# Kernel optimization log

Hardware: AMD Instinct MI355X
Metric: run time of the kernel (lower is better)

## Reference

```python
import jax, jax.numpy as jnp
import numpy as np

B, C, H, W = 8, 256, 64, 64
IC = 64  # inter_channels


def conv1x1(x, w, b):
    # x: [B,C,H,W], w: [O,C], b: [O]
    return jnp.einsum('bchw,oc->bohw', x, w) + b[None, :, None, None]


def maxpool2(x):
    # 2x2 max pool, stride 2. x: [B,C,H,W]
    b, c, h, w = x.shape
    return x.reshape(b, c, h // 2, 2, w // 2, 2).max(axis=(3, 5))


def setup_inputs() -> dict:
    key = jax.random.key(0)
    ks = jax.random.split(key, 9)
    s_in = 1.0 / np.sqrt(C)
    s_ic = 1.0 / np.sqrt(IC)
    return {
        'x': jax.random.normal(ks[0], (B, C, H, W), dtype=jnp.float32),
        'g_w': jax.random.uniform(ks[1], (IC, C), jnp.float32, -s_in, s_in),
        'g_b': jax.random.uniform(ks[2], (IC,), jnp.float32, -s_in, s_in),
        'theta_w': jax.random.uniform(ks[3], (IC, C), jnp.float32, -s_in, s_in),
        'theta_b': jax.random.uniform(ks[4], (IC,), jnp.float32, -s_in, s_in),
        'phi_w': jax.random.uniform(ks[5], (IC, C), jnp.float32, -s_in, s_in),
        'phi_b': jax.random.uniform(ks[6], (IC,), jnp.float32, -s_in, s_in),
        'W_w': jax.random.uniform(ks[7], (C, IC), jnp.float32, -np.sqrt(6.0 / IC), np.sqrt(6.0 / IC)),
        'W_b': jax.random.uniform(ks[8], (C,), jnp.float32, -s_ic, s_ic),
    }


def reference(x, g_w, g_b, theta_w, theta_b, phi_w, phi_b, W_w, W_b):
    b, c, h, w = x.shape
    n = h * w                     # query positions
    m = (h // 2) * (w // 2)       # pooled key/value positions

    v = maxpool2(conv1x1(x, g_w, g_b)).reshape(b, IC, m).transpose(0, 2, 1)   # [b,m,ic]
    q = conv1x1(x, theta_w, theta_b).reshape(b, IC, n).transpose(0, 2, 1)     # [b,n,ic]
    k = maxpool2(conv1x1(x, phi_w, phi_b)).reshape(b, IC, m)                  # [b,ic,m]

    attn = jax.nn.softmax(jnp.einsum('bni,bim->bnm', q, k), axis=-1)          # [b,n,m]
    attended = jnp.einsum('bnm,bmi->bni', attn, v)                            # [b,n,ic]
    attended = attended.transpose(0, 2, 1).reshape(b, IC, h, w)
    # F.interpolate to (h,w) is identity here: attended already has spatial (h,w)
    return conv1x1(attended, W_w, W_b) + x
```

## Files before the change

### kernel.cpp

```cpp
#include <hip/hip_runtime.h>

typedef unsigned short ushort_t;
typedef unsigned int   uint_t;

typedef __attribute__((ext_vector_type(8))) short  short8;
typedef __attribute__((ext_vector_type(4))) short  short4v;
typedef __attribute__((ext_vector_type(4))) float  float4v;

#define BB    8
#define CC    256
#define HH    64
#define WW2   64
#define NPIX  4096
#define MPOS  1024
#define ICH   64

__device__ __forceinline__ float bf2f(ushort_t u) {
  return __uint_as_float(((uint_t)u) << 16);
}
__device__ __forceinline__ ushort_t f2bf(float f) {
  uint_t i = __float_as_uint(f);
  uint_t r = (i + 0x7FFFu + ((i >> 16) & 1u)) >> 16;
  return (ushort_t)r;
}
__device__ __forceinline__ uint_t pack2(float a, float b) {
  return (uint_t)f2bf(a) | ((uint_t)f2bf(b) << 16);
}

__global__ __launch_bounds__(256) void prep_kernel(
    const float* __restrict__ theta_w, const float* __restrict__ phi_w,
    const float* __restrict__ g_w, const float* __restrict__ W_w,
    const float* __restrict__ theta_b, const float* __restrict__ phi_b,
    const float* __restrict__ g_b,
    ushort_t* __restrict__ wAll, ushort_t* __restrict__ Wbf,
    float* __restrict__ biasAll) {
  int i = blockIdx.x * 256 + threadIdx.x;
  if (i < 16384)        wAll[i] = f2bf(theta_w[i]);
  else if (i < 32768)   wAll[i] = f2bf(phi_w[i - 16384]);
  else if (i < 49152)   wAll[i] = f2bf(g_w[i - 32768]);
  else if (i < 65536)   Wbf[i - 49152] = f2bf(W_w[i - 49152]);
  else if (i < 65600)   biasAll[i - 65536] = theta_b[i - 65536];
  else if (i < 65664)   biasAll[i - 65536] = phi_b[i - 65600];
  else if (i < 65728)   biasAll[i - 65536] = g_b[i - 65664];
}

__global__ __launch_bounds__(256, 2) void qkv_kernel(
    const float* __restrict__ x, const ushort_t* __restrict__ wAll,
    const float* __restrict__ biasAll,
    ushort_t* __restrict__ qbuf, ushort_t* __restrict__ kTbuf,
    ushort_t* __restrict__ vTbuf) {
  __shared__ __align__(16) ushort_t Bs[2][64 * 64];
  int tid = threadIdx.x;
  int wave = tid >> 6, lane = tid & 63;
  int quad = lane >> 4, col = lane & 15;
  int b = blockIdx.x >> 6, tile = blockIdx.x & 63;
  int r2 = tile >> 1, chalf = tile & 1;
  const float* xb = x + (size_t)b * (CC * NPIX) + (r2 * 2) * WW2 + chalf * 32;

  int sp = tid & 63;
  int cq = tid >> 6;
  int goff = (sp >> 5) * WW2 + (sp & 31);

  float4v acc[3][4];
#pragma unroll
  for (int ot = 0; ot < 3; ++ot) {
    int ob = wave * 48 + ot * 16 + quad * 4;
    float4v bv;
#pragma unroll
    for (int r = 0; r < 4; ++r) bv[r] = biasAll[ob + r];
#pragma unroll
    for (int s = 0; s < 4; ++s) acc[ot][s] = bv;
  }

  float st[16];

#define LOAD_CHUNK(kc)                                                     \
  {                                                                        \
    _Pragma("unroll") for (int j = 0; j < 16; ++j)                         \
      st[j] = xb[((kc) * 64 + cq * 16 + j) * NPIX + goff];                 \
  }
#define WRITE_CHUNK(buf)                                                   \
  {                                                                        \
    _Pragma("unroll") for (int u = 0; u < 2; ++u) {                        \
      uint4 w;                                                             \
      w.x = pack2(st[u * 8 + 0], st[u * 8 + 1]);                           \
      w.y = pack2(st[u * 8 + 2], st[u * 8 + 3]);                           \
      w.z = pack2(st[u * 8 + 4], st[u * 8 + 5]);                           \
      w.w = pack2(st[u * 8 + 6], st[u * 8 + 7]);                           \
      *(uint4*)&Bs[(buf)][sp * 64 + (((cq * 2 + u) ^ (sp & 7)) * 8)] = w;  \
    }                                                                      \
  }

  LOAD_CHUNK(0);
  WRITE_CHUNK(0);
  __syncthreads();

  for (int kc = 0; kc < 4; ++kc) {
    if (kc < 3) LOAD_CHUNK(kc + 1);
    int buf = kc & 1;
#pragma unroll
    for (int ksl = 0; ksl < 2; ++ksl) {
      short8 aw[3];
#pragma unroll
      for (int ot = 0; ot < 3; ++ot)
        aw[ot] = *(const short8*)&wAll[(size_t)(wave * 48 + ot * 16 + col) * 256 +
                                       kc * 64 + ksl * 32 + quad * 8];
#pragma unroll
      for (int s = 0; s < 4; ++s) {
        short8 bx = *(const short8*)&Bs[buf][(s * 16 + col) * 64 +
                                             (((ksl * 4 + quad) ^ (col & 7)) * 8)];
#pragma unroll
        for (int ot = 0; ot < 3; ++ot)
          acc[ot][s] = __builtin_amdgcn_mfma_f32_16x16x32_bf16(aw[ot], bx, acc[ot][s], 0, 0, 0);
      }
    }
    if (kc < 3) {
      WRITE_CHUNK((kc + 1) & 1);
      __syncthreads();
    }
  }
#undef LOAD_CHUNK
#undef WRITE_CHUNK

#pragma unroll
  for (int ot = 0; ot < 3; ++ot) {
    int ob = wave * 48 + ot * 16;
    if (ob < 64) {
#pragma unroll
      for (int s = 0; s < 4; ++s) {
        int n = (r2 * 2 + (s >> 1)) * WW2 + chalf * 32 + (s & 1) * 16 + col;
        uint2 u;
        u.x = pack2(acc[ot][s][0], acc[ot][s][1]);
        u.y = pack2(acc[ot][s][2], acc[ot][s][3]);
        *(uint2*)&qbuf[((size_t)(b * NPIX + n)) * ICH + ob + quad * 4] = u;
      }
    } else if (ob < 128) {
#pragma unroll
      for (int s = 0; s < 2; ++s) {
        float4v pm;
#pragma unroll
        for (int r = 0; r < 4; ++r) {
          float v = fmaxf(acc[ot][s][r], acc[ot][s + 2][r]);
          pm[r] = fmaxf(v, __shfl_xor(v, 1));
        }
        if ((lane & 1) == 0) {
          int m = r2 * 32 + chalf * 16 + s * 8 + (col >> 1);
          uint2 u;
          u.x = pack2(pm[0], pm[1]);
          u.y = pack2(pm[2], pm[3]);
          *(uint2*)&kTbuf[((size_t)(b * MPOS + m)) * ICH + (ob - 64) + quad * 4] = u;
        }
      }
    } else {
#pragma unroll
      for (int s = 0; s < 2; ++s) {
        float4v pm;
#pragma unroll
        for (int r = 0; r < 4; ++r) {
          float v = fmaxf(acc[ot][s][r], acc[ot][s + 2][r]);
          pm[r] = fmaxf(v, __shfl_xor(v, 1));
        }
        if ((lane & 1) == 0) {
          int m = r2 * 32 + chalf * 16 + s * 8 + (col >> 1);
#pragma unroll
          for (int r = 0; r < 4; ++r)
            vTbuf[((size_t)(b * ICH + (ob - 128) + quad * 4 + r)) * MPOS + m] = f2bf(pm[r]);
        }
      }
    }
  }
}

__global__ __launch_bounds__(256, 2) void attn_kernel(
    const ushort_t* __restrict__ qbuf, const ushort_t* __restrict__ kTbuf,
    const ushort_t* __restrict__ vTbuf, ushort_t* __restrict__ attbuf) {
  __shared__ __align__(16) ushort_t Ks[2][64 * 64];
  __shared__ __align__(16) ushort_t Vs[2][64 * 64];
  __shared__ __align__(16) ushort_t Ps[64 * 68];
  int tid  = threadIdx.x;
  int wave = tid >> 6, lane = tid & 63;
  int quad = lane >> 4, col = lane & 15;
  int b = blockIdx.x >> 6, qt = blockIdx.x & 63;

  const ushort_t* qrow = qbuf + ((size_t)(b * NPIX + qt * 64 + wave * 16 + col)) * ICH;
  short8 aQ0 = *(const short8*)&qrow[quad * 8];
  short8 aQ1 = *(const short8*)&qrow[32 + quad * 8];

  int krow0 = tid >> 3,           kblk0 = tid & 7;
  int krow1 = (tid + 256) >> 3,   kblk1 = tid & 7;
  int vic = tid >> 2, vseg = tid & 3;

  const uint4* ksrc0 = (const uint4*)(kTbuf + ((size_t)(b * MPOS)) * ICH);
  const ushort_t* vbase = vTbuf + ((size_t)(b * ICH + vic)) * MPOS;

  {
    uint4 k0 = ksrc0[tid], k1 = ksrc0[tid + 256];
    const uint4* vsrc = (const uint4*)(vbase + vseg * 16);
    uint4 v0 = vsrc[0], v1 = vsrc[1];
    *(uint4*)&Ks[0][krow0 * 64 + ((kblk0 ^ (krow0 & 7)) * 8)] = k0;
    *(uint4*)&Ks[0][krow1 * 64 + ((kblk1 ^ (krow1 & 7)) * 8)] = k1;
    *(uint4*)&Vs[0][vic * 64 + (((vseg * 2 + 0) ^ (vic & 7)) * 8)] = v0;
    *(uint4*)&Vs[0][vic * 64 + (((vseg * 2 + 1) ^ (vic & 7)) * 8)] = v1;
  }
  __syncthreads();

  const float4v zero4 = {0.f, 0.f, 0.f, 0.f};
  float l_lane[4] = {0.f, 0.f, 0.f, 0.f};
  float4v o_acc[4];
#pragma unroll
  for (int t = 0; t < 4; ++t) o_acc[t] = zero4;

  for (int kt = 0; kt < 16; ++kt) {
    uint4 nk0, nk1, nv0, nv1;
    if (kt < 15) {
      const uint4* ksrc = (const uint4*)(kTbuf + ((size_t)(b * MPOS + (kt + 1) * 64)) * ICH);
      nk0 = ksrc[tid];
      nk1 = ksrc[tid + 256];
      const uint4* vsrc = (const uint4*)(vbase + (kt + 1) * 64 + vseg * 16);
      nv0 = vsrc[0];
      nv1 = vsrc[1];
    }
    int buf = kt & 1;

    float4v s_acc[4];
#pragma unroll
    for (int t = 0; t < 4; ++t) {
      float4v s = zero4;
      short8 bk0 = *(const short8*)&Ks[buf][(t * 16 + col) * 64 + (((0 * 4 + quad) ^ (col & 7)) * 8)];
      s = __builtin_amdgcn_mfma_f32_16x16x32_bf16(aQ0, bk0, s, 0, 0, 0);
      short8 bk1 = *(const short8*)&Ks[buf][(t * 16 + col) * 64 + (((1 * 4 + quad) ^ (col & 7)) * 8)];
      s = __builtin_amdgcn_mfma_f32_16x16x32_bf16(aQ1, bk1, s, 0, 0, 0);
      s_acc[t] = s;
    }

#pragma unroll
    for (int r = 0; r < 4; ++r) {
      int prow = (wave * 16 + quad * 4 + r) * 68;
#pragma unroll
      for (int t = 0; t < 4; ++t) {
        float pv = __expf(s_acc[t][r]);
        l_lane[r] += pv;
        Ps[prow + t * 16 + col] = f2bf(pv);
      }
    }

#pragma unroll
    for (int kk = 0; kk < 2; ++kk) {
      int pbase = (wave * 16 + col) * 68 + kk * 32 + quad * 8;
      short4v plo = *(const short4v*)&Ps[pbase];
      short4v phi = *(const short4v*)&Ps[pbase + 4];
      short8 ap = __builtin_shufflevector(plo, phi, 0, 1, 2, 3, 4, 5, 6, 7);
#pragma unroll
      for (int t = 0; t < 4; ++t) {
        short8 bv = *(const short8*)&Vs[buf][(t * 16 + col) * 64 + (((kk * 4 + quad) ^ (col & 7)) * 8)];
        o_acc[t] = __builtin_amdgcn_mfma_f32_16x16x32_bf16(ap, bv, o_acc[t], 0, 0, 0);
      }
    }

    if (kt < 15) {
      int nbuf = buf ^ 1;
      *(uint4*)&Ks[nbuf][krow0 * 64 + ((kblk0 ^ (krow0 & 7)) * 8)] = nk0;
      *(uint4*)&Ks[nbuf][krow1 * 64 + ((kblk1 ^ (krow1 & 7)) * 8)] = nk1;
      *(uint4*)&Vs[nbuf][vic * 64 + (((vseg * 2 + 0) ^ (vic & 7)) * 8)] = nv0;
      *(uint4*)&Vs[nbuf][vic * 64 + (((vseg * 2 + 1) ^ (vic & 7)) * 8)] = nv1;
      __syncthreads();
    }
  }

#pragma unroll
  for (int r = 0; r < 4; ++r) {
    float l = l_lane[r];
    l += __shfl_xor(l, 1);
    l += __shfl_xor(l, 2);
    l += __shfl_xor(l, 4);
    l += __shfl_xor(l, 8);
    float inv = 1.0f / l;
    size_t row = ((size_t)(b * NPIX + qt * 64 + wave * 16 + quad * 4 + r)) * ICH;
#pragma unroll
    for (int t = 0; t < 4; ++t)
      attbuf[row + t * 16 + col] = f2bf(o_acc[t][r] * inv);
  }
}

__global__ __launch_bounds__(256, 2) void outconv_kernel(
    const ushort_t* __restrict__ attbuf, const float* __restrict__ x,
    const ushort_t* __restrict__ Wbf, const float* __restrict__ W_b,
    float* __restrict__ out) {
  int tid = threadIdx.x;
  int wave = tid >> 6, lane = tid & 63;
  int quad = lane >> 4, col = lane & 15;
  int b = blockIdx.x >> 6, pt = blockIdx.x & 63;

  float4v acc[4][4];
#pragma unroll
  for (int os = 0; os < 4; ++os) {
    float bv = W_b[wave * 64 + os * 16 + col];
    float4v bvec = {bv, bv, bv, bv};
#pragma unroll
    for (int ps = 0; ps < 4; ++ps) acc[os][ps] = bvec;
  }

  short8 af[2][4];
#pragma unroll
  for (int ps = 0; ps < 4; ++ps)
#pragma unroll
    for (int ks = 0; ks < 2; ++ks)
      af[ks][ps] = *(const short8*)&attbuf[((size_t)(b * NPIX + pt * 64 + ps * 16 + col)) * ICH +
                                           ks * 32 + quad * 8];

#pragma unroll
  for (int os = 0; os < 4; ++os) {
#pragma unroll
    for (int ks = 0; ks < 2; ++ks) {
      short8 wf = *(const short8*)&Wbf[(size_t)(wave * 64 + os * 16 + col) * ICH +
                                       ks * 32 + quad * 8];
#pragma unroll
      for (int ps = 0; ps < 4; ++ps)
        acc[os][ps] = __builtin_amdgcn_mfma_f32_16x16x32_bf16(af[ks][ps], wf, acc[os][ps], 0, 0, 0);
    }
  }

#pragma unroll
  for (int os = 0; os < 4; ++os) {
#pragma unroll
    for (int ps = 0; ps < 4; ++ps) {
      int o = wave * 64 + os * 16 + col;
      int p = pt * 64 + ps * 16 + quad * 4;
      size_t idx = ((size_t)(b * CC + o)) * NPIX + p;
      float4 xv = *(const float4*)&x[idx];
      float4 ov;
      ov.x = acc[os][ps][0] + xv.x;
      ov.y = acc[os][ps][1] + xv.y;
      ov.z = acc[os][ps][2] + xv.z;
      ov.w = acc[os][ps][3] + xv.w;
      *(float4*)&out[idx] = ov;
    }
  }
}

extern "C" void kernel_launch(void* const* d_in, const int* in_sizes, int n_in,
                              void* d_out, int out_size, void* d_ws, size_t ws_size,
                              hipStream_t stream) {
  const float* x       = (const float*)d_in[0];
  const float* g_w     = (const float*)d_in[1];
  const float* g_b     = (const float*)d_in[2];
  const float* theta_w = (const float*)d_in[3];
  const float* theta_b = (const float*)d_in[4];
  const float* phi_w   = (const float*)d_in[5];
  const float* phi_b   = (const float*)d_in[6];
  const float* W_w     = (const float*)d_in[7];
  const float* W_b     = (const float*)d_in[8];
  (void)in_sizes; (void)n_in; (void)out_size; (void)ws_size;

  char* ws = (char*)d_ws;
  ushort_t* wAll    = (ushort_t*)(ws + 0);
  ushort_t* Wbf     = (ushort_t*)(ws + 98304);
  float*    biasAll = (float*)(ws + 131072);
  ushort_t* qbuf    = (ushort_t*)(ws + 262144);
  ushort_t* kTbuf   = (ushort_t*)(ws + 4456448);
  ushort_t* vTbuf   = (ushort_t*)(ws + 5505024);
  ushort_t* attbuf  = (ushort_t*)(ws + 6553600);
  float* out = (float*)d_out;

  prep_kernel<<<257, 256, 0, stream>>>(theta_w, phi_w, g_w, W_w,
                                       theta_b, phi_b, g_b,
                                       wAll, Wbf, biasAll);
  qkv_kernel<<<512, 256, 0, stream>>>(x, wAll, biasAll, qbuf, kTbuf, vTbuf);
  attn_kernel<<<512, 256, 0, stream>>>(qbuf, kTbuf, vTbuf, attbuf);
  outconv_kernel<<<512, 256, 0, stream>>>(attbuf, x, Wbf, W_b, out);
}
```

Before: 135.4 us.

## Pre-transpose x to bf16, split attention keys across waves, double grid sizes

A new prep kernel transposes x into a pixel-major bf16 buffer, so the QKV projection can read MFMA operands straight from global memory with no LDS staging. The attention kernel now gives each block 32 queries, with two wave pairs handling the two key halves; their partial outputs and row sums are combined through shared memory at the end. The QKV, attention and output-conv kernels all launch twice as many smaller blocks with higher occupancy hints. The cost is an extra full pass that writes and re-reads a transposed copy of x, more synchronisation in the attention loop, and the P matrix is now rounded with a cheaper round-half-away mode.

```diff
diff --git a/kernel.cpp b/kernel.cpp
--- a/kernel.cpp
+++ b/kernel.cpp
@@ -23,155 +23,143 @@
   uint_t r = (i + 0x7FFFu + ((i >> 16) & 1u)) >> 16;
   return (ushort_t)r;
 }
+__device__ __forceinline__ ushort_t f2bf_rna(float f) {
+  return (ushort_t)((__float_as_uint(f) + 0x8000u) >> 16);
+}
 __device__ __forceinline__ uint_t pack2(float a, float b) {
   return (uint_t)f2bf(a) | ((uint_t)f2bf(b) << 16);
 }
 
-__global__ __launch_bounds__(256) void prep_kernel(
+__global__ __launch_bounds__(256) void xpose_prep_kernel(
+    const float* __restrict__ x,
     const float* __restrict__ theta_w, const float* __restrict__ phi_w,
     const float* __restrict__ g_w, const float* __restrict__ W_w,
     const float* __restrict__ theta_b, const float* __restrict__ phi_b,
     const float* __restrict__ g_b,
-    ushort_t* __restrict__ wAll, ushort_t* __restrict__ Wbf,
-    float* __restrict__ biasAll) {
-  int i = blockIdx.x * 256 + threadIdx.x;
-  if (i < 16384)        wAll[i] = f2bf(theta_w[i]);
-  else if (i < 32768)   wAll[i] = f2bf(phi_w[i - 16384]);
-  else if (i < 49152)   wAll[i] = f2bf(g_w[i - 32768]);
-  else if (i < 65536)   Wbf[i - 49152] = f2bf(W_w[i - 49152]);
-  else if (i < 65600)   biasAll[i - 65536] = theta_b[i - 65536];
-  else if (i < 65664)   biasAll[i - 65536] = phi_b[i - 65600];
-  else if (i < 65728)   biasAll[i - 65536] = g_b[i - 65664];
-}
-
-__global__ __launch_bounds__(256, 2) void qkv_kernel(
-    const float* __restrict__ x, const ushort_t* __restrict__ wAll,
+    ushort_t* __restrict__ xT, ushort_t* __restrict__ wAll,
+    ushort_t* __restrict__ Wbf, float* __restrict__ biasAll) {
+  int bid = blockIdx.x;
+  int tid = threadIdx.x;
+  if (bid < 2048) {
+    __shared__ __align__(16) ushort_t T[64 * 72];
+    int b = bid >> 8, rest = bid & 255;
+    int ct = rest >> 6, pt = rest & 63;
+    int w = tid >> 6, pl = tid & 63;
+    const float* src = x + ((size_t)(b * CC + ct * 64)) * NPIX + pt * 64;
+#pragma unroll
+    for (int i = 0; i < 16; ++i) {
+      int cl = i * 4 + w;
+      T[pl * 72 + cl] = f2bf(src[(size_t)cl * NPIX + pl]);
+    }
+    __syncthreads();
+#pragma unroll
+    for (int j = 0; j < 2; ++j) {
+      int flat = tid * 2 + j;
+      int p = flat >> 3, seg = flat & 7;
+      uint4 v = *(const uint4*)&T[p * 72 + seg * 8];
+      *(uint4*)&xT[((size_t)(b * NPIX + pt * 64 + p)) * CC + ct * 64 + seg * 8] = v;
+    }
+  } else {
+    int i = (bid - 2048) * 256 + tid;
+    if (i < 16384)        wAll[i] = f2bf(theta_w[i]);
+    else if (i < 32768)   wAll[i] = f2bf(phi_w[i - 16384]);
+    else if (i < 49152)   wAll[i] = f2bf(g_w[i - 32768]);
+    else if (i < 65536)   Wbf[i - 49152] = f2bf(W_w[i - 49152]);
+    else if (i < 65600)   biasAll[i - 65536] = theta_b[i - 65536];
+    else if (i < 65664)   biasAll[i - 65536] = phi_b[i - 65600];
+    else if (i < 65728)   biasAll[i - 65536] = g_b[i - 65664];
+  }
+}
+
+__global__ __launch_bounds__(256, 4) void qkv_kernel(
+    const ushort_t* __restrict__ xT, const ushort_t* __restrict__ wAll,
     const float* __restrict__ biasAll,
     ushort_t* __restrict__ qbuf, ushort_t* __restrict__ kTbuf,
     ushort_t* __restrict__ vTbuf) {
-  __shared__ __align__(16) ushort_t Bs[2][64 * 64];
   int tid = threadIdx.x;
   int wave = tid >> 6, lane = tid & 63;
   int quad = lane >> 4, col = lane & 15;
-  int b = blockIdx.x >> 6, tile = blockIdx.x & 63;
-  int r2 = tile >> 1, chalf = tile & 1;
-  const float* xb = x + (size_t)b * (CC * NPIX) + (r2 * 2) * WW2 + chalf * 32;
-
-  int sp = tid & 63;
-  int cq = tid >> 6;
-  int goff = (sp >> 5) * WW2 + (sp & 31);
-
-  float4v acc[3][4];
+  int b = blockIdx.x >> 7, tile = blockIdx.x & 127;
+  int r2 = tile >> 2, co = tile & 3;
+
+  const ushort_t* brow0 = xT + ((size_t)(b * NPIX + (2 * r2 + 0) * WW2 + co * 16 + col)) * CC;
+  const ushort_t* brow1 = xT + ((size_t)(b * NPIX + (2 * r2 + 1) * WW2 + co * 16 + col)) * CC;
+  const ushort_t* wbase = wAll + (size_t)(wave * 48 + col) * CC;
+
+  float4v acc[3][2];
 #pragma unroll
   for (int ot = 0; ot < 3; ++ot) {
     int ob = wave * 48 + ot * 16 + quad * 4;
     float4v bv;
 #pragma unroll
     for (int r = 0; r < 4; ++r) bv[r] = biasAll[ob + r];
-#pragma unroll
-    for (int s = 0; s < 4; ++s) acc[ot][s] = bv;
-  }
-
-  float st[16];
-
-#define LOAD_CHUNK(kc)                                                     \
-  {                                                                        \
-    _Pragma("unroll") for (int j = 0; j < 16; ++j)                         \
-      st[j] = xb[((kc) * 64 + cq * 16 + j) * NPIX + goff];                 \
-  }
-#define WRITE_CHUNK(buf)                                                   \
-  {                                                                        \
-    _Pragma("unroll") for (int u = 0; u < 2; ++u) {                        \
-      uint4 w;                                                             \
-      w.x = pack2(st[u * 8 + 0], st[u * 8 + 1]);                           \
-      w.y = pack2(st[u * 8 + 2], st[u * 8 + 3]);                           \
-      w.z = pack2(st[u * 8 + 4], st[u * 8 + 5]);                           \
-      w.w = pack2(st[u * 8 + 6], st[u * 8 + 7]);                           \
-      *(uint4*)&Bs[(buf)][sp * 64 + (((cq * 2 + u) ^ (sp & 7)) * 8)] = w;  \
-    }                                                                      \
-  }
-
-  LOAD_CHUNK(0);
-  WRITE_CHUNK(0);
-  __syncthreads();
-
+    acc[ot][0] = bv;
+    acc[ot][1] = bv;
+  }
+
+#pragma unroll
   for (int kc = 0; kc < 4; ++kc) {
-    if (kc < 3) LOAD_CHUNK(kc + 1);
-    int buf = kc & 1;
 #pragma unroll
     for (int ksl = 0; ksl < 2; ++ksl) {
+      int koff = kc * 64 + ksl * 32 + quad * 8;
       short8 aw[3];
 #pragma unroll
       for (int ot = 0; ot < 3; ++ot)
-        aw[ot] = *(const short8*)&wAll[(size_t)(wave * 48 + ot * 16 + col) * 256 +
-                                       kc * 64 + ksl * 32 + quad * 8];
-#pragma unroll
-      for (int s = 0; s < 4; ++s) {
-        short8 bx = *(const short8*)&Bs[buf][(s * 16 + col) * 64 +
-                                             (((ksl * 4 + quad) ^ (col & 7)) * 8)];
-#pragma unroll
-        for (int ot = 0; ot < 3; ++ot)
-          acc[ot][s] = __builtin_amdgcn_mfma_f32_16x16x32_bf16(aw[ot], bx, acc[ot][s], 0, 0, 0);
-      }
-    }
-    if (kc < 3) {
-      WRITE_CHUNK((kc + 1) & 1);
-      __syncthreads();
-    }
-  }
-#undef LOAD_CHUNK
-#undef WRITE_CHUNK
+        aw[ot] = *(const short8*)&wbase[(size_t)(ot * 16) * CC + koff];
+      short8 b0 = *(const short8*)&brow0[koff];
+      short8 b1 = *(const short8*)&brow1[koff];
+#pragma unroll
+      for (int ot = 0; ot < 3; ++ot) {
+        acc[ot][0] = __builtin_amdgcn_mfma_f32_16x16x32_bf16(aw[ot], b0, acc[ot][0], 0, 0, 0);
+        acc[ot][1] = __builtin_amdgcn_mfma_f32_16x16x32_bf16(aw[ot], b1, acc[ot][1], 0, 0, 0);
+      }
+    }
+  }
 
 #pragma unroll
   for (int ot = 0; ot < 3; ++ot) {
     int ob = wave * 48 + ot * 16;
     if (ob < 64) {
 #pragma unroll
-      for (int s = 0; s < 4; ++s) {
-        int n = (r2 * 2 + (s >> 1)) * WW2 + chalf * 32 + (s & 1) * 16 + col;
+      for (int s = 0; s < 2; ++s) {
+        int n = (2 * r2 + s) * WW2 + co * 16 + col;
         uint2 u;
         u.x = pack2(acc[ot][s][0], acc[ot][s][1]);
         u.y = pack2(acc[ot][s][2], acc[ot][s][3]);
         *(uint2*)&qbuf[((size_t)(b * NPIX + n)) * ICH + ob + quad * 4] = u;
       }
     } else if (ob < 128) {
-#pragma unroll
-      for (int s = 0; s < 2; ++s) {
-        float4v pm;
-#pragma unroll
-        for (int r = 0; r < 4; ++r) {
-          float v = fmaxf(acc[ot][s][r], acc[ot][s + 2][r]);
-          pm[r] = fmaxf(v, __shfl_xor(v, 1));
-        }
-        if ((lane & 1) == 0) {
-          int m = r2 * 32 + chalf * 16 + s * 8 + (col >> 1);
-          uint2 u;
-          u.x = pack2(pm[0], pm[1]);
-          u.y = pack2(pm[2], pm[3]);
-          *(uint2*)&kTbuf[((size_t)(b * MPOS + m)) * ICH + (ob - 64) + quad * 4] = u;
-        }
+      float4v pm;
+#pragma unroll
+      for (int r = 0; r < 4; ++r) {
+        float v = fmaxf(acc[ot][0][r], acc[ot][1][r]);
+        pm[r] = fmaxf(v, __shfl_xor(v, 1));
+      }
+      if ((lane & 1) == 0) {
+        int m = r2 * 32 + co * 8 + (col >> 1);
+        uint2 u;
+        u.x = pack2(pm[0], pm[1]);
+        u.y = pack2(pm[2], pm[3]);
+        *(uint2*)&kTbuf[((size_t)(b * MPOS + m)) * ICH + (ob - 64) + quad * 4] = u;
       }
     } else {
-#pragma unroll
-      for (int s = 0; s < 2; ++s) {
-        float4v pm;
-#pragma unroll
-        for (int r = 0; r < 4; ++r) {
-          float v = fmaxf(acc[ot][s][r], acc[ot][s + 2][r]);
-          pm[r] = fmaxf(v, __shfl_xor(v, 1));
-        }
-        if ((lane & 1) == 0) {
-          int m = r2 * 32 + chalf * 16 + s * 8 + (col >> 1);
-#pragma unroll
-          for (int r = 0; r < 4; ++r)
-            vTbuf[((size_t)(b * ICH + (ob - 128) + quad * 4 + r)) * MPOS + m] = f2bf(pm[r]);
-        }
-      }
-    }
-  }
-}
-
-__global__ __launch_bounds__(256, 2) void attn_kernel(
+      float4v pm;
+#pragma unroll
+      for (int r = 0; r < 4; ++r) {
+        float v = fmaxf(acc[ot][0][r], acc[ot][1][r]);
+        pm[r] = fmaxf(v, __shfl_xor(v, 1));
+      }
+      if ((lane & 1) == 0) {
+        int m = r2 * 32 + co * 8 + (col >> 1);
+#pragma unroll
+        for (int r = 0; r < 4; ++r)
+          vTbuf[((size_t)(b * ICH + (ob - 128) + quad * 4 + r)) * MPOS + m] = f2bf(pm[r]);
+      }
+    }
+  }
+}
+
+__global__ __launch_bounds__(256, 3) void attn_kernel(
     const ushort_t* __restrict__ qbuf, const ushort_t* __restrict__ kTbuf,
     const ushort_t* __restrict__ vTbuf, ushort_t* __restrict__ attbuf) {
   __shared__ __align__(16) ushort_t Ks[2][64 * 64];
@@ -180,28 +168,45 @@
   int tid  = threadIdx.x;
   int wave = tid >> 6, lane = tid & 63;
   int quad = lane >> 4, col = lane & 15;
-  int b = blockIdx.x >> 6, qt = blockIdx.x & 63;
-
-  const ushort_t* qrow = qbuf + ((size_t)(b * NPIX + qt * 64 + wave * 16 + col)) * ICH;
+  int wq = wave & 1, wk = wave >> 1;
+  int b = blockIdx.x >> 7, qt = blockIdx.x & 127;
+
+  const ushort_t* qrow = qbuf + ((size_t)(b * NPIX + qt * 32 + wq * 16 + col)) * ICH;
   short8 aQ0 = *(const short8*)&qrow[quad * 8];
   short8 aQ1 = *(const short8*)&qrow[32 + quad * 8];
 
-  int krow0 = tid >> 3,           kblk0 = tid & 7;
-  int krow1 = (tid + 256) >> 3,   kblk1 = tid & 7;
+  int krow0 = tid >> 3, kblk = tid & 7;
+  int krow1 = krow0 + 32;
   int vic = tid >> 2, vseg = tid & 3;
-
-  const uint4* ksrc0 = (const uint4*)(kTbuf + ((size_t)(b * MPOS)) * ICH);
+  const uint4* kbase = (const uint4*)(kTbuf + ((size_t)(b * MPOS)) * ICH);
   const ushort_t* vbase = vTbuf + ((size_t)(b * ICH + vic)) * MPOS;
 
-  {
-    uint4 k0 = ksrc0[tid], k1 = ksrc0[tid + 256];
-    const uint4* vsrc = (const uint4*)(vbase + vseg * 16);
-    uint4 v0 = vsrc[0], v1 = vsrc[1];
-    *(uint4*)&Ks[0][krow0 * 64 + ((kblk0 ^ (krow0 & 7)) * 8)] = k0;
-    *(uint4*)&Ks[0][krow1 * 64 + ((kblk1 ^ (krow1 & 7)) * 8)] = k1;
-    *(uint4*)&Vs[0][vic * 64 + (((vseg * 2 + 0) ^ (vic & 7)) * 8)] = v0;
-    *(uint4*)&Vs[0][vic * 64 + (((vseg * 2 + 1) ^ (vic & 7)) * 8)] = v1;
-  }
+  uint4 pk[4], pv[4];
+#define AT_LOAD(i)                                                          \
+  {                                                                         \
+    const uint4* k0p = kbase + (size_t)(i) * 512;                           \
+    const uint4* k1p = kbase + (size_t)((i) + 8) * 512;                     \
+    pk[0] = k0p[tid]; pk[1] = k0p[tid + 256];                               \
+    pk[2] = k1p[tid]; pk[3] = k1p[tid + 256];                               \
+    const uint4* v0p = (const uint4*)(vbase + (i) * 64);                    \
+    const uint4* v1p = (const uint4*)(vbase + ((i) + 8) * 64);              \
+    pv[0] = v0p[vseg]; pv[1] = v0p[vseg + 4];                               \
+    pv[2] = v1p[vseg]; pv[3] = v1p[vseg + 4];                               \
+  }
+#define AT_WRITE()                                                          \
+  {                                                                         \
+    *(uint4*)&Ks[0][krow0 * 64 + ((kblk ^ (krow0 & 7)) * 8)] = pk[0];       \
+    *(uint4*)&Ks[0][krow1 * 64 + ((kblk ^ (krow1 & 7)) * 8)] = pk[1];       \
+    *(uint4*)&Ks[1][krow0 * 64 + ((kblk ^ (krow0 & 7)) * 8)] = pk[2];       \
+    *(uint4*)&Ks[1][krow1 * 64 + ((kblk ^ (krow1 & 7)) * 8)] = pk[3];       \
+    *(uint4*)&Vs[0][vic * 64 + ((vseg ^ (vic & 7)) * 8)] = pv[0];           \
+    *(uint4*)&Vs[0][vic * 64 + (((vseg + 4) ^ (vic & 7)) * 8)] = pv[1];     \
+    *(uint4*)&Vs[1][vic * 64 + ((vseg ^ (vic & 7)) * 8)] = pv[2];           \
+    *(uint4*)&Vs[1][vic * 64 + (((vseg + 4) ^ (vic & 7)) * 8)] = pv[3];     \
+  }
+
+  AT_LOAD(0);
+  AT_WRITE();
   __syncthreads();
 
   const float4v zero4 = {0.f, 0.f, 0.f, 0.f};
@@ -210,25 +215,16 @@
 #pragma unroll
   for (int t = 0; t < 4; ++t) o_acc[t] = zero4;
 
-  for (int kt = 0; kt < 16; ++kt) {
-    uint4 nk0, nk1, nv0, nv1;
-    if (kt < 15) {
-      const uint4* ksrc = (const uint4*)(kTbuf + ((size_t)(b * MPOS + (kt + 1) * 64)) * ICH);
-      nk0 = ksrc[tid];
-      nk1 = ksrc[tid + 256];
-      const uint4* vsrc = (const uint4*)(vbase + (kt + 1) * 64 + vseg * 16);
-      nv0 = vsrc[0];
-      nv1 = vsrc[1];
-    }
-    int buf = kt & 1;
+  for (int i = 0; i < 8; ++i) {
+    if (i < 7) AT_LOAD(i + 1);
 
     float4v s_acc[4];
 #pragma unroll
     for (int t = 0; t < 4; ++t) {
       float4v s = zero4;
-      short8 bk0 = *(const short8*)&Ks[buf][(t * 16 + col) * 64 + (((0 * 4 + quad) ^ (col & 7)) * 8)];
+      short8 bk0 = *(const short8*)&Ks[wk][(t * 16 + col) * 64 + ((quad ^ (col & 7)) * 8)];
       s = __builtin_amdgcn_mfma_f32_16x16x32_bf16(aQ0, bk0, s, 0, 0, 0);
-      short8 bk1 = *(const short8*)&Ks[buf][(t * 16 + col) * 64 + (((1 * 4 + quad) ^ (col & 7)) * 8)];
+      short8 bk1 = *(const short8*)&Ks[wk][(t * 16 + col) * 64 + (((4 + quad) ^ (col & 7)) * 8)];
       s = __builtin_amdgcn_mfma_f32_16x16x32_bf16(aQ1, bk1, s, 0, 0, 0);
       s_acc[t] = s;
     }
@@ -238,9 +234,9 @@
       int prow = (wave * 16 + quad * 4 + r) * 68;
 #pragma unroll
       for (int t = 0; t < 4; ++t) {
-        float pv = __expf(s_acc[t][r]);
-        l_lane[r] += pv;
-        Ps[prow + t * 16 + col] = f2bf(pv);
+        float pv_ = __expf(s_acc[t][r]);
+        l_lane[r] += pv_;
+        Ps[prow + t * 16 + col] = f2bf_rna(pv_);
       }
     }
 
@@ -252,60 +248,78 @@
       short8 ap = __builtin_shufflevector(plo, phi, 0, 1, 2, 3, 4, 5, 6, 7);
 #pragma unroll
       for (int t = 0; t < 4; ++t) {
-        short8 bv = *(const short8*)&Vs[buf][(t * 16 + col) * 64 + (((kk * 4 + quad) ^ (col & 7)) * 8)];
+        short8 bv = *(const short8*)&Vs[wk][(t * 16 + col) * 64 + (((kk * 4 + quad) ^ (col & 7)) * 8)];
         o_acc[t] = __builtin_amdgcn_mfma_f32_16x16x32_bf16(ap, bv, o_acc[t], 0, 0, 0);
       }
     }
 
-    if (kt < 15) {
-      int nbuf = buf ^ 1;
-      *(uint4*)&Ks[nbuf][krow0 * 64 + ((kblk0 ^ (krow0 & 7)) * 8)] = nk0;
-      *(uint4*)&Ks[nbuf][krow1 * 64 + ((kblk1 ^ (krow1 & 7)) * 8)] = nk1;
-      *(uint4*)&Vs[nbuf][vic * 64 + (((vseg * 2 + 0) ^ (vic & 7)) * 8)] = nv0;
-      *(uint4*)&Vs[nbuf][vic * 64 + (((vseg * 2 + 1) ^ (vic & 7)) * 8)] = nv1;
+    if (i < 7) {
       __syncthreads();
-    }
-  }
-
-#pragma unroll
-  for (int r = 0; r < 4; ++r) {
-    float l = l_lane[r];
-    l += __shfl_xor(l, 1);
-    l += __shfl_xor(l, 2);
-    l += __shfl_xor(l, 4);
-    l += __shfl_xor(l, 8);
-    float inv = 1.0f / l;
-    size_t row = ((size_t)(b * NPIX + qt * 64 + wave * 16 + quad * 4 + r)) * ICH;
+      AT_WRITE();
+      __syncthreads();
+    }
+  }
+#undef AT_LOAD
+#undef AT_WRITE
+
+  __syncthreads();
+  float* S = (float*)Ks;
+  if (wk == 1) {
+    float* dst = S + (size_t)(wq * 64 + lane) * 20;
 #pragma unroll
     for (int t = 0; t < 4; ++t)
-      attbuf[row + t * 16 + col] = f2bf(o_acc[t][r] * inv);
-  }
-}
-
-__global__ __launch_bounds__(256, 2) void outconv_kernel(
+#pragma unroll
+      for (int r = 0; r < 4; ++r) dst[t * 4 + r] = o_acc[t][r];
+#pragma unroll
+    for (int r = 0; r < 4; ++r) dst[16 + r] = l_lane[r];
+  }
+  __syncthreads();
+  if (wk == 0) {
+    const float* srcp = S + (size_t)(wq * 64 + lane) * 20;
+#pragma unroll
+    for (int t = 0; t < 4; ++t)
+#pragma unroll
+      for (int r = 0; r < 4; ++r) o_acc[t][r] += srcp[t * 4 + r];
+#pragma unroll
+    for (int r = 0; r < 4; ++r) {
+      float l = l_lane[r] + srcp[16 + r];
+      l += __shfl_xor(l, 1);
+      l += __shfl_xor(l, 2);
+      l += __shfl_xor(l, 4);
+      l += __shfl_xor(l, 8);
+      float inv = 1.0f / l;
+      size_t row = ((size_t)(b * NPIX + qt * 32 + wq * 16 + quad * 4 + r)) * ICH;
+#pragma unroll
+      for (int t = 0; t < 4; ++t)
+        attbuf[row + t * 16 + col] = f2bf(o_acc[t][r] * inv);
+    }
+  }
+}
+
+__global__ __launch_bounds__(256, 4) void outconv_kernel(
     const ushort_t* __restrict__ attbuf, const float* __restrict__ x,
     const ushort_t* __restrict__ Wbf, const float* __restrict__ W_b,
     float* __restrict__ out) {
   int tid = threadIdx.x;
   int wave = tid >> 6, lane = tid & 63;
   int quad = lane >> 4, col = lane & 15;
-  int b = blockIdx.x >> 6, pt = blockIdx.x & 63;
-
-  float4v acc[4][4];
+  int b = blockIdx.x >> 7, pt = blockIdx.x & 127;
+
+  float4v acc[4][2];
 #pragma unroll
   for (int os = 0; os < 4; ++os) {
     float bv = W_b[wave * 64 + os * 16 + col];
     float4v bvec = {bv, bv, bv, bv};
-#pragma unroll
-    for (int ps = 0; ps < 4; ++ps) acc[os][ps] = bvec;
-  }
-
-  short8 af[2][4];
-#pragma unroll
-  for (int ps = 0; ps < 4; ++ps)
+    acc[os][0] = bvec;
+    acc[os][1] = bvec;
+  }
+
+  short8 af[2][2];
+#pragma unroll
+  for (int ps = 0; ps < 2; ++ps)
 #pragma unroll
     for (int ks = 0; ks < 2; ++ks)
-      af[ks][ps] = *(const short8*)&attbuf[((size_t)(b * NPIX + pt * 64 + ps * 16 + col)) * ICH +
+      af[ks][ps] = *(const short8*)&attbuf[((size_t)(b * NPIX + pt * 32 + ps * 16 + col)) * ICH +
                                            ks * 32 + quad * 8];
 
 #pragma unroll
@@ -314,18 +328,17 @@
     for (int ks = 0; ks < 2; ++ks) {
       short8 wf = *(const short8*)&Wbf[(size_t)(wave * 64 + os * 16 + col) * ICH +
                                        ks * 32 + quad * 8];
-#pragma unroll
-      for (int ps = 0; ps < 4; ++ps)
-        acc[os][ps] = __builtin_amdgcn_mfma_f32_16x16x32_bf16(af[ks][ps], wf, acc[os][ps], 0, 0, 0);
+      acc[os][0] = __builtin_amdgcn_mfma_f32_16x16x32_bf16(af[ks][0], wf, acc[os][0], 0, 0, 0);
+      acc[os][1] = __builtin_amdgcn_mfma_f32_16x16x32_bf16(af[ks][1], wf, acc[os][1], 0, 0, 0);
     }
   }
 
 #pragma unroll
   for (int os = 0; os < 4; ++os) {
 #pragma unroll
-    for (int ps = 0; ps < 4; ++ps) {
+    for (int ps = 0; ps < 2; ++ps) {
       int o = wave * 64 + os * 16 + col;
-      int p = pt * 64 + ps * 16 + quad * 4;
+      int p = pt * 32 + ps * 16 + quad * 4;
       size_t idx = ((size_t)(b * CC + o)) * NPIX + p;
       float4 xv = *(const float4*)&x[idx];
       float4 ov;
@@ -356,16 +369,17 @@
   ushort_t* wAll    = (ushort_t*)(ws + 0);
   ushort_t* Wbf     = (ushort_t*)(ws + 98304);
   float*    biasAll = (float*)(ws + 131072);
-  ushort_t* qbuf    = (ushort_t*)(ws + 262144);
-  ushort_t* kTbuf   = (ushort_t*)(ws + 4456448);
-  ushort_t* vTbuf   = (ushort_t*)(ws + 5505024);
-  ushort_t* attbuf  = (ushort_t*)(ws + 6553600);
+  ushort_t* xT      = (ushort_t*)(ws + 262144);
+  ushort_t* attbuf  = (ushort_t*)(ws + 262144);
+  ushort_t* qbuf    = (ushort_t*)(ws + 17039360);
+  ushort_t* kTbuf   = (ushort_t*)(ws + 21233664);
+  ushort_t* vTbuf   = (ushort_t*)(ws + 22282240);
   float* out = (float*)d_out;
 
-  prep_kernel<<<257, 256, 0, stream>>>(theta_w, phi_w, g_w, W_w,
-                                       theta_b, phi_b, g_b,
-                                       wAll, Wbf, biasAll);
-  qkv_kernel<<<512, 256, 0, stream>>>(x, wAll, biasAll, qbuf, kTbuf, vTbuf);
-  attn_kernel<<<512, 256, 0, stream>>>(qbuf, kTbuf, vTbuf, attbuf);
-  outconv_kernel<<<512, 256, 0, stream>>>(attbuf, x, Wbf, W_b, out);
-}
+  xpose_prep_kernel<<<2305, 256, 0, stream>>>(x, theta_w, phi_w, g_w, W_w,
+                                              theta_b, phi_b, g_b,
+                                              xT, wAll, Wbf, biasAll);
+  qkv_kernel<<<1024, 256, 0, stream>>>(xT, wAll, biasAll, qbuf, kTbuf, vTbuf);
+  attn_kernel<<<1024, 256, 0, stream>>>(qbuf, kTbuf, vTbuf, attbuf);
+  outconv_kernel<<<1024, 256, 0, stream>>>(attbuf, x, Wbf, W_b, out);
+}
```

Result: slower. 210.4 us (+55.4%).

## Pre-transpose x to pixel-major bf16 and re-tile qkv and outconv kernels

Applied to the files above, without the earlier changes.

A new prep kernel transposes x into a pixel-major bf16 buffer and stores the weights in a k-block-interleaved layout. The qkv kernel then loads a whole 64x256 tile into LDS with coalesced 16-byte loads instead of strided fp32 gathers. It raises occupancy to 4 blocks per SM, and the output conv uses smaller 32-pixel tiles across twice as many blocks. Softmax probabilities now use a cheaper round-to-nearest bf16 conversion. The trade-off is an extra full read and write of x through the transpose buffer.

```diff
diff --git a/kernel.cpp b/kernel.cpp
--- a/kernel.cpp
+++ b/kernel.cpp
@@ -23,43 +23,85 @@
   uint_t r = (i + 0x7FFFu + ((i >> 16) & 1u)) >> 16;
   return (ushort_t)r;
 }
+__device__ __forceinline__ ushort_t f2bf_rna(float f) {
+  return (ushort_t)((__float_as_uint(f) + 0x8000u) >> 16);
+}
 __device__ __forceinline__ uint_t pack2(float a, float b) {
   return (uint_t)f2bf(a) | ((uint_t)f2bf(b) << 16);
 }
 
-__global__ __launch_bounds__(256) void prep_kernel(
+__global__ __launch_bounds__(256) void xpose_prep_kernel(
+    const float* __restrict__ x,
     const float* __restrict__ theta_w, const float* __restrict__ phi_w,
     const float* __restrict__ g_w, const float* __restrict__ W_w,
     const float* __restrict__ theta_b, const float* __restrict__ phi_b,
     const float* __restrict__ g_b,
-    ushort_t* __restrict__ wAll, ushort_t* __restrict__ Wbf,
-    float* __restrict__ biasAll) {
-  int i = blockIdx.x * 256 + threadIdx.x;
-  if (i < 16384)        wAll[i] = f2bf(theta_w[i]);
-  else if (i < 32768)   wAll[i] = f2bf(phi_w[i - 16384]);
-  else if (i < 49152)   wAll[i] = f2bf(g_w[i - 32768]);
-  else if (i < 65536)   Wbf[i - 49152] = f2bf(W_w[i - 49152]);
-  else if (i < 65600)   biasAll[i - 65536] = theta_b[i - 65536];
-  else if (i < 65664)   biasAll[i - 65536] = phi_b[i - 65600];
-  else if (i < 65728)   biasAll[i - 65536] = g_b[i - 65664];
-}
-
-__global__ __launch_bounds__(256, 2) void qkv_kernel(
-    const float* __restrict__ x, const ushort_t* __restrict__ wAll,
+    ushort_t* __restrict__ xT, ushort_t* __restrict__ wA2,
+    ushort_t* __restrict__ Wbf2, float* __restrict__ biasAll) {
+  int bid = blockIdx.x;
+  int tid = threadIdx.x;
+  if (bid < 2048) {
+    __shared__ __align__(16) ushort_t T[64 * 72];
+    int b = bid >> 8, rest = bid & 255;
+    int ct = rest >> 6, pt = rest & 63;
+    int w = tid >> 6, pl = tid & 63;
+    const float* src = x + ((size_t)(b * CC + ct * 64)) * NPIX + pt * 64;
+#pragma unroll
+    for (int i = 0; i < 16; ++i) {
+      int cl = i * 4 + w;
+      T[pl * 72 + cl] = f2bf(src[(size_t)cl * NPIX + pl]);
+    }
+    __syncthreads();
+#pragma unroll
+    for (int j = 0; j < 2; ++j) {
+      int flat = tid * 2 + j;
+      int p = flat >> 3, seg = flat & 7;
+      uint4 v = *(const uint4*)&T[p * 72 + seg * 8];
+      *(uint4*)&xT[((size_t)(b * NPIX + pt * 64 + p)) * CC + ct * 64 + seg * 8] = v;
+    }
+  } else {
+    int i = (bid - 2048) * 256 + tid;
+    if (i < 49152) {
+      float v = (i < 16384) ? theta_w[i]
+              : (i < 32768) ? phi_w[i - 16384]
+                            : g_w[i - 32768];
+      int o = i >> 8, c = i & 255;
+      wA2[(c >> 3) * 1536 + o * 8 + (c & 7)] = f2bf(v);
+    } else if (i < 65536) {
+      int j = i - 49152;
+      int o = j >> 6, ic = j & 63;
+      Wbf2[(ic >> 3) * 2048 + o * 8 + (ic & 7)] = f2bf(W_w[j]);
+    } else if (i < 65600)    biasAll[i - 65536] = theta_b[i - 65536];
+    else if (i < 65664)      biasAll[i - 65536] = phi_b[i - 65600];
+    else if (i < 65728)      biasAll[i - 65536] = g_b[i - 65664];
+  }
+}
+
+__global__ __launch_bounds__(256, 4) void qkv_kernel(
+    const ushort_t* __restrict__ xT, const ushort_t* __restrict__ wA2,
     const float* __restrict__ biasAll,
     ushort_t* __restrict__ qbuf, ushort_t* __restrict__ kTbuf,
     ushort_t* __restrict__ vTbuf) {
-  __shared__ __align__(16) ushort_t Bs[2][64 * 64];
+  __shared__ __align__(16) ushort_t Bsu[64 * 256];
+  uint4* Bs16 = (uint4*)Bsu;
   int tid = threadIdx.x;
   int wave = tid >> 6, lane = tid & 63;
   int quad = lane >> 4, col = lane & 15;
-  int b = blockIdx.x >> 6, tile = blockIdx.x & 63;
-  int r2 = tile >> 1, chalf = tile & 1;
-  const float* xb = x + (size_t)b * (CC * NPIX) + (r2 * 2) * WW2 + chalf * 32;
-
-  int sp = tid & 63;
-  int cq = tid >> 6;
-  int goff = (sp >> 5) * WW2 + (sp & 31);
+  int b = blockIdx.x >> 6, t = blockIdx.x & 63;
+  int rj = t >> 1, h = t & 1;
+
+  const uint4* src0 = (const uint4*)(xT + ((size_t)(b * NPIX + (2 * rj + 0) * WW2 + h * 32)) * CC);
+  const uint4* src1 = (const uint4*)(xT + ((size_t)(b * NPIX + (2 * rj + 1) * WW2 + h * 32)) * CC);
+
+#pragma unroll
+  for (int it = 0; it < 8; ++it) {
+    int g = it * 256 + tid;
+    int chunk = g >> 10, off = g & 1023;
+    int lp = chunk * 32 + (off >> 5), j = off & 31;
+    uint4 v = (chunk == 0) ? src0[off] : src1[off];
+    Bs16[lp * 32 + (j & ~7) + ((j & 7) ^ (lp & 7))] = v;
+  }
+  __syncthreads();
 
   float4v acc[3][4];
 #pragma unroll
@@ -72,55 +114,26 @@
     for (int s = 0; s < 4; ++s) acc[ot][s] = bv;
   }
 
-  float st[16];
-
-#define LOAD_CHUNK(kc)                                                     \
-  {                                                                        \
-    _Pragma("unroll") for (int j = 0; j < 16; ++j)                         \
-      st[j] = xb[((kc) * 64 + cq * 16 + j) * NPIX + goff];                 \
-  }
-#define WRITE_CHUNK(buf)                                                   \
-  {                                                                        \
-    _Pragma("unroll") for (int u = 0; u < 2; ++u) {                        \
-      uint4 w;                                                             \
-      w.x = pack2(st[u * 8 + 0], st[u * 8 + 1]);                           \
-      w.y = pack2(st[u * 8 + 2], st[u * 8 + 3]);                           \
-      w.z = pack2(st[u * 8 + 4], st[u * 8 + 5]);                           \
-      w.w = pack2(st[u * 8 + 6], st[u * 8 + 7]);                           \
-      *(uint4*)&Bs[(buf)][sp * 64 + (((cq * 2 + u) ^ (sp & 7)) * 8)] = w;  \
-    }                                                                      \
-  }
-
-  LOAD_CHUNK(0);
-  WRITE_CHUNK(0);
-  __syncthreads();
-
-  for (int kc = 0; kc < 4; ++kc) {
-    if (kc < 3) LOAD_CHUNK(kc + 1);
-    int buf = kc & 1;
-#pragma unroll
-    for (int ksl = 0; ksl < 2; ++ksl) {
-      short8 aw[3];
+  const uint4* wA16 = (const uint4*)wA2;
+#pragma unroll
+  for (int ks = 0; ks < 8; ++ks) {
+    int kblk = ks * 4 + quad;
+    short8 aw[3];
+#pragma unroll
+    for (int ot = 0; ot < 3; ++ot) {
+      uint4 a = wA16[kblk * 192 + wave * 48 + ot * 16 + col];
+      aw[ot] = *(const short8*)&a;
+    }
+#pragma unroll
+    for (int s = 0; s < 4; ++s) {
+      int lp = s * 16 + col;
+      uint4 braw = Bs16[lp * 32 + (kblk & ~7) + ((kblk & 7) ^ (lp & 7))];
+      short8 bx = *(const short8*)&braw;
 #pragma unroll
       for (int ot = 0; ot < 3; ++ot)
-        aw[ot] = *(const short8*)&wAll[(size_t)(wave * 48 + ot * 16 + col) * 256 +
-                                       kc * 64 + ksl * 32 + quad * 8];
-#pragma unroll
-      for (int s = 0; s < 4; ++s) {
-        short8 bx = *(const short8*)&Bs[buf][(s * 16 + col) * 64 +
-                                             (((ksl * 4 + quad) ^ (col & 7)) * 8)];
-#pragma unroll
-        for (int ot = 0; ot < 3; ++ot)
-          acc[ot][s] = __builtin_amdgcn_mfma_f32_16x16x32_bf16(aw[ot], bx, acc[ot][s], 0, 0, 0);
-      }
-    }
-    if (kc < 3) {
-      WRITE_CHUNK((kc + 1) & 1);
-      __syncthreads();
-    }
-  }
-#undef LOAD_CHUNK
-#undef WRITE_CHUNK
+        acc[ot][s] = __builtin_amdgcn_mfma_f32_16x16x32_bf16(aw[ot], bx, acc[ot][s], 0, 0, 0);
+    }
+  }
 
 #pragma unroll
   for (int ot = 0; ot < 3; ++ot) {
@@ -128,7 +141,7 @@
     if (ob < 64) {
 #pragma unroll
       for (int s = 0; s < 4; ++s) {
-        int n = (r2 * 2 + (s >> 1)) * WW2 + chalf * 32 + (s & 1) * 16 + col;
+        int n = (2 * rj + (s >> 1)) * WW2 + h * 32 + (s & 1) * 16 + col;
         uint2 u;
         u.x = pack2(acc[ot][s][0], acc[ot][s][1]);
         u.y = pack2(acc[ot][s][2], acc[ot][s][3]);
@@ -144,7 +157,7 @@
           pm[r] = fmaxf(v, __shfl_xor(v, 1));
         }
         if ((lane & 1) == 0) {
-          int m = r2 * 32 + chalf * 16 + s * 8 + (col >> 1);
+          int m = rj * 32 + h * 16 + s * 8 + (col >> 1);
           uint2 u;
           u.x = pack2(pm[0], pm[1]);
           u.y = pack2(pm[2], pm[3]);
@@ -161,7 +174,7 @@
           pm[r] = fmaxf(v, __shfl_xor(v, 1));
         }
         if ((lane & 1) == 0) {
-          int m = r2 * 32 + chalf * 16 + s * 8 + (col >> 1);
+          int m = rj * 32 + h * 16 + s * 8 + (col >> 1);
 #pragma unroll
           for (int r = 0; r < 4; ++r)
             vTbuf[((size_t)(b * ICH + (ob - 128) + quad * 4 + r)) * MPOS + m] = f2bf(pm[r]);
@@ -226,9 +239,9 @@
 #pragma unroll
     for (int t = 0; t < 4; ++t) {
       float4v s = zero4;
-      short8 bk0 = *(const short8*)&Ks[buf][(t * 16 + col) * 64 + (((0 * 4 + quad) ^ (col & 7)) * 8)];
+      short8 bk0 = *(const short8*)&Ks[buf][(t * 16 + col) * 64 + ((quad ^ (col & 7)) * 8)];
       s = __builtin_amdgcn_mfma_f32_16x16x32_bf16(aQ0, bk0, s, 0, 0, 0);
-      short8 bk1 = *(const short8*)&Ks[buf][(t * 16 + col) * 64 + (((1 * 4 + quad) ^ (col & 7)) * 8)];
+      short8 bk1 = *(const short8*)&Ks[buf][(t * 16 + col) * 64 + (((4 + quad) ^ (col & 7)) * 8)];
       s = __builtin_amdgcn_mfma_f32_16x16x32_bf16(aQ1, bk1, s, 0, 0, 0);
       s_acc[t] = s;
     }
@@ -240,7 +253,7 @@
       for (int t = 0; t < 4; ++t) {
         float pv = __expf(s_acc[t][r]);
         l_lane[r] += pv;
-        Ps[prow + t * 16 + col] = f2bf(pv);
+        Ps[prow + t * 16 + col] = f2bf_rna(pv);
       }
     }
 
@@ -282,50 +295,50 @@
   }
 }
 
-__global__ __launch_bounds__(256, 2) void outconv_kernel(
+__global__ __launch_bounds__(256, 4) void outconv_kernel(
     const ushort_t* __restrict__ attbuf, const float* __restrict__ x,
-    const ushort_t* __restrict__ Wbf, const float* __restrict__ W_b,
+    const ushort_t* __restrict__ Wbf2, const float* __restrict__ W_b,
     float* __restrict__ out) {
   int tid = threadIdx.x;
   int wave = tid >> 6, lane = tid & 63;
   int quad = lane >> 4, col = lane & 15;
-  int b = blockIdx.x >> 6, pt = blockIdx.x & 63;
-
-  float4v acc[4][4];
+  int b = blockIdx.x >> 7, pt = blockIdx.x & 127;
+
+  float4v acc[4][2];
 #pragma unroll
   for (int os = 0; os < 4; ++os) {
     float bv = W_b[wave * 64 + os * 16 + col];
     float4v bvec = {bv, bv, bv, bv};
-#pragma unroll
-    for (int ps = 0; ps < 4; ++ps) acc[os][ps] = bvec;
-  }
-
-  short8 af[2][4];
-#pragma unroll
-  for (int ps = 0; ps < 4; ++ps)
+    acc[os][0] = bvec;
+    acc[os][1] = bvec;
+  }
+
+  short8 af[2][2];
+#pragma unroll
+  for (int ps = 0; ps < 2; ++ps)
 #pragma unroll
     for (int ks = 0; ks < 2; ++ks)
-      af[ks][ps] = *(const short8*)&attbuf[((size_t)(b * NPIX + pt * 64 + ps * 16 + col)) * ICH +
+      af[ks][ps] = *(const short8*)&attbuf[((size_t)(b * NPIX + pt * 32 + ps * 16 + col)) * ICH +
                                            ks * 32 + quad * 8];
 
+  const uint4* W16 = (const uint4*)Wbf2;
 #pragma unroll
   for (int os = 0; os < 4; ++os) {
 #pragma unroll
     for (int ks = 0; ks < 2; ++ks) {
-      short8 wf = *(const short8*)&Wbf[(size_t)(wave * 64 + os * 16 + col) * ICH +
-                                       ks * 32 + quad * 8];
-#pragma unroll
-      for (int ps = 0; ps < 4; ++ps)
-        acc[os][ps] = __builtin_amdgcn_mfma_f32_16x16x32_bf16(af[ks][ps], wf, acc[os][ps], 0, 0, 0);
+      uint4 wr = W16[(ks * 4 + quad) * 256 + wave * 64 + os * 16 + col];
+      short8 wf = *(const short8*)&wr;
+      acc[os][0] = __builtin_amdgcn_mfma_f32_16x16x32_bf16(af[ks][0], wf, acc[os][0], 0, 0, 0);
+      acc[os][1] = __builtin_amdgcn_mfma_f32_16x16x32_bf16(af[ks][1], wf, acc[os][1], 0, 0, 0);
     }
   }
 
 #pragma unroll
   for (int os = 0; os < 4; ++os) {
 #pragma unroll
-    for (int ps = 0; ps < 4; ++ps) {
+    for (int ps = 0; ps < 2; ++ps) {
       int o = wave * 64 + os * 16 + col;
-      int p = pt * 64 + ps * 16 + quad * 4;
+      int p = pt * 32 + ps * 16 + quad * 4;
       size_t idx = ((size_t)(b * CC + o)) * NPIX + p;
       float4 xv = *(const float4*)&x[idx];
       float4 ov;
@@ -353,19 +366,20 @@
   (void)in_sizes; (void)n_in; (void)out_size; (void)ws_size;
 
   char* ws = (char*)d_ws;
-  ushort_t* wAll    = (ushort_t*)(ws + 0);
-  ushort_t* Wbf     = (ushort_t*)(ws + 98304);
+  ushort_t* wA2     = (ushort_t*)(ws + 0);
+  ushort_t* Wbf2    = (ushort_t*)(ws + 98304);
   float*    biasAll = (float*)(ws + 131072);
-  ushort_t* qbuf    = (ushort_t*)(ws + 262144);
-  ushort_t* kTbuf   = (ushort_t*)(ws + 4456448);
-  ushort_t* vTbuf   = (ushort_t*)(ws + 5505024);
-  ushort_t* attbuf  = (ushort_t*)(ws + 6553600);
+  ushort_t* xT      = (ushort_t*)(ws + 262144);
+  ushort_t* attbuf  = (ushort_t*)(ws + 262144);
+  ushort_t* qbuf    = (ushort_t*)(ws + 17039360);
+  ushort_t* kTbuf   = (ushort_t*)(ws + 21233664);
+  ushort_t* vTbuf   = (ushort_t*)(ws + 22282240);
   float* out = (float*)d_out;
 
-  prep_kernel<<<257, 256, 0, stream>>>(theta_w, phi_w, g_w, W_w,
-                                       theta_b, phi_b, g_b,
-                                       wAll, Wbf, biasAll);
-  qkv_kernel<<<512, 256, 0, stream>>>(x, wAll, biasAll, qbuf, kTbuf, vTbuf);
+  xpose_prep_kernel<<<2305, 256, 0, stream>>>(x, theta_w, phi_w, g_w, W_w,
+                                              theta_b, phi_b, g_b,
+                                              xT, wA2, Wbf2, biasAll);
+  qkv_kernel<<<512, 256, 0, stream>>>(xT, wA2, biasAll, qbuf, kTbuf, vTbuf);
   attn_kernel<<<512, 256, 0, stream>>>(qbuf, kTbuf, vTbuf, attbuf);
-  outconv_kernel<<<512, 256, 0, stream>>>(attbuf, x, Wbf, W_b, out);
-}
+  outconv_kernel<<<1024, 256, 0, stream>>>(attbuf, x, Wbf2, W_b, out);
+}
```

Result: slower. 139.0 us (+2.7%).
